# Performance work log

Hardware: AMD Instinct MI355X
Metric: run time of the kernel (lower is better)

Reference implementation:

```python
import jax, jax.numpy as jnp
import numpy as np

B, T, F = 512, 256, 1024


def setup_inputs() -> dict:
    key = jax.random.key(0)
    ks = jax.random.split(key, 8)
    s = 1.0 / np.sqrt(F)
    return {
        "z_state": jax.random.normal(ks[0], (B, F), dtype=jnp.float32),
        "past_predictions": jax.random.normal(ks[1], (B, T, F), dtype=jnp.float32),
        "Wq": jax.random.normal(ks[2], (F, F), dtype=jnp.float32) * s,
        "Wk": jax.random.normal(ks[3], (F, F), dtype=jnp.float32) * s,
        "Wv": jax.random.normal(ks[4], (F, F), dtype=jnp.float32) * s,
        "bq": jnp.zeros((F,), dtype=jnp.float32),
        "bk": jnp.zeros((F,), dtype=jnp.float32),
        "bv": jnp.zeros((F,), dtype=jnp.float32),
    }


def reference(z_state, past_predictions, Wq, Wk, Wv, bq, bk, bv):
    # torch Linear: y = x @ W.T + b  (W is [out, in])
    query = z_state @ Wq.T + bq                         # [B, D]
    keys = jnp.einsum("btf,df->btd", past_predictions, Wk) + bk   # [B, T, D]
    values = jnp.einsum("btf,df->btd", past_predictions, Wv) + bv  # [B, T, D]
    # single-query attention: scores [B, T] (note: no 1/sqrt(d) scaling in source)
    scores = jnp.einsum("bd,btd->bt", query, keys)
    weights = jax.nn.softmax(scores, axis=-1)
    context = jnp.einsum("bt,btd->bd", weights, values)  # [B, D]
    return context
```

## Files before the change

kernel.cpp:

```cpp
#include <hip/hip_runtime.h>
#include <math.h>


#define MM 512
#define NN 1024
#define KK 1024

template<int BT, int SUMA, int BIAS>
__global__ __launch_bounds__(256) void gemm_f32(const float* __restrict__ A,
        const float* __restrict__ Bm, const float* __restrict__ bias,
        float* __restrict__ C)
{
    __shared__ float As[16][68];
    __shared__ float Bs[16][68];
    const int tid = threadIdx.x;
    const int tx = tid & 15, ty = tid >> 4;
    const int n0 = blockIdx.x * 64, m0 = blockIdx.y * 64, kz = blockIdx.z;
    const int kbeg = kz * 512;
    const int arow = tid >> 2, akq = tid & 3;

    float c[4][4] = {};

    for (int kt = 0; kt < 512; kt += 16) {
        const int k0 = kbeg + kt;
        {
            const float* ap = A + (size_t)(m0 + arow) * KK + k0 + akq * 4;
            float4 a = *(const float4*)ap;
            if (SUMA) {
                float4 a2 = *(const float4*)(ap + MM * NN);
                a.x += a2.x; a.y += a2.y; a.z += a2.z; a.w += a2.w;
            }
            As[akq*4+0][arow] = a.x; As[akq*4+1][arow] = a.y;
            As[akq*4+2][arow] = a.z; As[akq*4+3][arow] = a.w;
        }
        if (BT) {
            const float* bp = Bm + (size_t)(n0 + arow) * KK + k0 + akq * 4;
            float4 b = *(const float4*)bp;
            Bs[akq*4+0][arow] = b.x; Bs[akq*4+1][arow] = b.y;
            Bs[akq*4+2][arow] = b.z; Bs[akq*4+3][arow] = b.w;
        } else {
            const int krow = tid >> 4, nq = tid & 15;
            float4 b = *(const float4*)(Bm + (size_t)(k0 + krow) * NN + n0 + nq * 4);
            *(float4*)&Bs[krow][nq * 4] = b;
        }
        __syncthreads();
        #pragma unroll
        for (int k = 0; k < 16; ++k) {
            float4 a4 = *(const float4*)&As[k][ty * 4];
            float4 b4 = *(const float4*)&Bs[k][tx * 4];
            float av[4] = {a4.x, a4.y, a4.z, a4.w};
            float bw[4] = {b4.x, b4.y, b4.z, b4.w};
            #pragma unroll
            for (int i = 0; i < 4; ++i)
                #pragma unroll
                for (int j = 0; j < 4; ++j)
                    c[i][j] = fmaf(av[i], bw[j], c[i][j]);
        }
        __syncthreads();
    }

    float* Cp = C + (size_t)kz * MM * NN;
    #pragma unroll
    for (int i = 0; i < 4; ++i) {
        const int m = m0 + ty * 4 + i;
        const int n = n0 + tx * 4;
        float4 o = make_float4(c[i][0], c[i][1], c[i][2], c[i][3]);
        if (BIAS && kz == 0) {
            o.x += bias[n]; o.y += bias[n+1]; o.z += bias[n+2]; o.w += bias[n+3];
        }
        *(float4*)&Cp[(size_t)m * NN + n] = o;
    }
}

__global__ __launch_bounds__(256) void attn_stream(const float* __restrict__ past,
        const float* __restrict__ qk2, float* __restrict__ ctx)
{
    const int b = blockIdx.x;
    const int e = threadIdx.x;
    const int lane = e & 63, w = e >> 6;
    __shared__ float red[2][4][8];

    const float* qp = qk2 + (size_t)b * 1024 + e * 4;
    float4 q4 = *(const float4*)qp;
    {
        float4 q4b = *(const float4*)(qp + MM * NN);
        q4.x += q4b.x; q4.y += q4b.y; q4.z += q4b.z; q4.w += q4b.w;
    }

    float4 acc = make_float4(0.f, 0.f, 0.f, 0.f);
    float m = -INFINITY, l = 0.f;
    const float* base = past + (size_t)b * 256 * 1024 + e * 4;

    for (int t0 = 0; t0 < 256; t0 += 8) {
        const int buf = (t0 >> 3) & 1;
        float4 r[8];
        float p[8];
        #pragma unroll
        for (int j = 0; j < 8; ++j)
            r[j] = *(const float4*)(base + (size_t)(t0 + j) * 1024);
        #pragma unroll
        for (int j = 0; j < 8; ++j)
            p[j] = q4.x*r[j].x + q4.y*r[j].y + q4.z*r[j].z + q4.w*r[j].w;
        #pragma unroll
        for (int j = 0; j < 8; ++j) {
            #pragma unroll
            for (int off = 1; off < 64; off <<= 1)
                p[j] += __shfl_xor(p[j], off, 64);
        }
        if (lane == 0) {
            #pragma unroll
            for (int j = 0; j < 8; ++j) red[buf][w][j] = p[j];
        }
        __syncthreads();
        float s[8];
        #pragma unroll
        for (int j = 0; j < 8; ++j)
            s[j] = red[buf][0][j] + red[buf][1][j] + red[buf][2][j] + red[buf][3][j];

        float cmax = s[0];
        #pragma unroll
        for (int j = 1; j < 8; ++j) cmax = fmaxf(cmax, s[j]);
        const float mn = fmaxf(m, cmax);
        const float alpha = __expf(m - mn);
        float pe[8], sum = 0.f;
        #pragma unroll
        for (int j = 0; j < 8; ++j) { pe[j] = __expf(s[j] - mn); sum += pe[j]; }
        l = l * alpha + sum;
        acc.x *= alpha; acc.y *= alpha; acc.z *= alpha; acc.w *= alpha;
        #pragma unroll
        for (int j = 0; j < 8; ++j) {
            acc.x = fmaf(pe[j], r[j].x, acc.x);
            acc.y = fmaf(pe[j], r[j].y, acc.y);
            acc.z = fmaf(pe[j], r[j].z, acc.z);
            acc.w = fmaf(pe[j], r[j].w, acc.w);
        }
        m = mn;
    }
    const float inv = 1.0f / l;
    float4 o = make_float4(acc.x * inv, acc.y * inv, acc.z * inv, acc.w * inv);
    *(float4*)(ctx + (size_t)b * 1024 + e * 4) = o;
}

__global__ __launch_bounds__(256) void add_bias_out(const float* __restrict__ o2,
        const float* __restrict__ bv, float* __restrict__ out)
{
    const int i = (blockIdx.x * 256 + threadIdx.x) * 4;
    float4 a = *(const float4*)(o2 + i);
    float4 b = *(const float4*)(o2 + MM * NN + i);
    const int n = i & 1023;
    float4 bb = *(const float4*)(bv + n);
    float4 r = make_float4(a.x + b.x + bb.x, a.y + b.y + bb.y,
                           a.z + b.z + bb.z, a.w + b.w + bb.w);
    *(float4*)(out + i) = r;
}

extern "C" void kernel_launch(void* const* d_in, const int* in_sizes, int n_in,
                              void* d_out, int out_size, void* d_ws, size_t ws_size,
                              hipStream_t stream) {
    const float* z    = (const float*)d_in[0];
    const float* past = (const float*)d_in[1];
    const float* Wq   = (const float*)d_in[2];
    const float* Wk   = (const float*)d_in[3];
    const float* Wv   = (const float*)d_in[4];
    const float* bq   = (const float*)d_in[5];
    const float* bv   = (const float*)d_in[7];
    float* out = (float*)d_out;

    float* q2  = (float*)d_ws;
    float* qk2 = q2 + 2 * MM * NN;
    float* ctx = qk2 + 2 * MM * NN;
    float* o2  = q2;

    dim3 g(NN / 64, MM / 64, 2), blk(256);
    gemm_f32<1, 0, 1><<<g, blk, 0, stream>>>(z,   Wq, bq,      q2);
    gemm_f32<0, 1, 0><<<g, blk, 0, stream>>>(q2,  Wk, nullptr, qk2);
    attn_stream<<<dim3(512), blk, 0, stream>>>(past, qk2, ctx);
    gemm_f32<1, 0, 0><<<g, blk, 0, stream>>>(ctx, Wv, nullptr, o2);
    add_bias_out<<<dim3(512), blk, 0, stream>>>(o2, bv, out);
}
```

Baseline: 795.5 us.

## Split attention over time across wavefronts with split-K combine and wider GEMM K-split

Replaces the one-block-per-batch streaming attention with a split-T design: 2048 blocks, each wavefront handling 16 timesteps independently with a lazy-rescale online softmax and no block-level syncs. A separate combine kernel merges the per-wave partial (m, l, acc) results. The GEMM K-split also rises from 2 to 4 partitions to launch more blocks. The cost is extra partial-result traffic (about 32MB of pacc) and more reduction reads in the consumer kernels.

```diff
diff --git a/kernel.cpp b/kernel.cpp
--- a/kernel.cpp
+++ b/kernel.cpp
@@ -5,6 +5,8 @@
 #define MM 512
 #define NN 1024
 #define KK 1024
+#define NPART 4
+#define KCHUNK (KK / NPART)
 
 template<int BT, int SUMA, int BIAS>
 __global__ __launch_bounds__(256) void gemm_f32(const float* __restrict__ A,
@@ -16,19 +18,22 @@
     const int tid = threadIdx.x;
     const int tx = tid & 15, ty = tid >> 4;
     const int n0 = blockIdx.x * 64, m0 = blockIdx.y * 64, kz = blockIdx.z;
-    const int kbeg = kz * 512;
+    const int kbeg = kz * KCHUNK;
     const int arow = tid >> 2, akq = tid & 3;
 
     float c[4][4] = {};
 
-    for (int kt = 0; kt < 512; kt += 16) {
+    for (int kt = 0; kt < KCHUNK; kt += 16) {
         const int k0 = kbeg + kt;
         {
             const float* ap = A + (size_t)(m0 + arow) * KK + k0 + akq * 4;
             float4 a = *(const float4*)ap;
             if (SUMA) {
-                float4 a2 = *(const float4*)(ap + MM * NN);
-                a.x += a2.x; a.y += a2.y; a.z += a2.z; a.w += a2.w;
+                #pragma unroll
+                for (int p = 1; p < NPART; ++p) {
+                    float4 a2 = *(const float4*)(ap + (size_t)p * MM * NN);
+                    a.x += a2.x; a.y += a2.y; a.z += a2.z; a.w += a2.w;
+                }
             }
             As[akq*4+0][arow] = a.x; As[akq*4+1][arow] = a.y;
             As[akq*4+2][arow] = a.z; As[akq*4+3][arow] = a.w;
@@ -72,73 +77,117 @@
     }
 }
 
-__global__ __launch_bounds__(256) void attn_stream(const float* __restrict__ past,
-        const float* __restrict__ qk2, float* __restrict__ ctx)
+#define TW 16
+
+__global__ __launch_bounds__(256) void attn_part(const float* __restrict__ past,
+        const float* __restrict__ qk2, float* __restrict__ pacc,
+        float2* __restrict__ pml)
+{
+    const int bid = blockIdx.x;
+    const int b = bid >> 2, c = bid & 3;
+    const int lane = threadIdx.x & 63, w = threadIdx.x >> 6;
+    const int widx = (c << 2) | w;
+    const int t0 = widx * TW;
+
+    float4 qk[4];
+    #pragma unroll
+    for (int q = 0; q < 4; ++q) {
+        const float* qp = qk2 + (size_t)b * NN + q * 256 + lane * 4;
+        float4 v = *(const float4*)qp;
+        #pragma unroll
+        for (int p = 1; p < NPART; ++p) {
+            float4 v2 = *(const float4*)(qp + (size_t)p * MM * NN);
+            v.x += v2.x; v.y += v2.y; v.z += v2.z; v.w += v2.w;
+        }
+        qk[q] = v;
+    }
+
+    const float* base = past + ((size_t)b * 256 + t0) * NN + lane * 4;
+    float m = -INFINITY, l = 0.f;
+    float4 acc[4] = {};
+
+    float4 r[4], rn[4];
+    #pragma unroll
+    for (int q = 0; q < 4; ++q) r[q] = *(const float4*)(base + q * 256);
+
+    #pragma unroll 2
+    for (int t = 0; t < TW; ++t) {
+        if (t + 1 < TW) {
+            #pragma unroll
+            for (int q = 0; q < 4; ++q)
+                rn[q] = *(const float4*)(base + (size_t)(t + 1) * NN + q * 256);
+        }
+        const float d0 = r[0].x*qk[0].x + r[0].y*qk[0].y + r[0].z*qk[0].z + r[0].w*qk[0].w;
+        const float d1 = r[1].x*qk[1].x + r[1].y*qk[1].y + r[1].z*qk[1].z + r[1].w*qk[1].w;
+        const float d2 = r[2].x*qk[2].x + r[2].y*qk[2].y + r[2].z*qk[2].z + r[2].w*qk[2].w;
+        const float d3 = r[3].x*qk[3].x + r[3].y*qk[3].y + r[3].z*qk[3].z + r[3].w*qk[3].w;
+        float p = (d0 + d1) + (d2 + d3);
+        #pragma unroll
+        for (int off = 1; off < 64; off <<= 1)
+            p += __shfl_xor(p, off, 64);
+        float dd = p - m;
+        if (dd > 8.f) {
+            const float alpha = __expf(-dd);
+            l *= alpha;
+            #pragma unroll
+            for (int q = 0; q < 4; ++q) {
+                acc[q].x *= alpha; acc[q].y *= alpha;
+                acc[q].z *= alpha; acc[q].w *= alpha;
+            }
+            m = p; dd = 0.f;
+        }
+        const float pe = __expf(dd);
+        l += pe;
+        #pragma unroll
+        for (int q = 0; q < 4; ++q) {
+            acc[q].x = fmaf(pe, r[q].x, acc[q].x);
+            acc[q].y = fmaf(pe, r[q].y, acc[q].y);
+            acc[q].z = fmaf(pe, r[q].z, acc[q].z);
+            acc[q].w = fmaf(pe, r[q].w, acc[q].w);
+        }
+        #pragma unroll
+        for (int q = 0; q < 4; ++q) r[q] = rn[q];
+    }
+
+    float* pa = pacc + ((size_t)b * 16 + widx) * NN + lane * 4;
+    #pragma unroll
+    for (int q = 0; q < 4; ++q) *(float4*)(pa + q * 256) = acc[q];
+    if (lane == 0) pml[b * 16 + widx] = make_float2(m, l);
+}
+
+__global__ __launch_bounds__(256) void attn_combine(const float* __restrict__ pacc,
+        const float2* __restrict__ pml, float* __restrict__ ctx)
 {
     const int b = blockIdx.x;
     const int e = threadIdx.x;
-    const int lane = e & 63, w = e >> 6;
-    __shared__ float red[2][4][8];
-
-    const float* qp = qk2 + (size_t)b * 1024 + e * 4;
-    float4 q4 = *(const float4*)qp;
-    {
-        float4 q4b = *(const float4*)(qp + MM * NN);
-        q4.x += q4b.x; q4.y += q4b.y; q4.z += q4b.z; q4.w += q4b.w;
-    }
-
-    float4 acc = make_float4(0.f, 0.f, 0.f, 0.f);
-    float m = -INFINITY, l = 0.f;
-    const float* base = past + (size_t)b * 256 * 1024 + e * 4;
-
-    for (int t0 = 0; t0 < 256; t0 += 8) {
-        const int buf = (t0 >> 3) & 1;
-        float4 r[8];
-        float p[8];
-        #pragma unroll
-        for (int j = 0; j < 8; ++j)
-            r[j] = *(const float4*)(base + (size_t)(t0 + j) * 1024);
-        #pragma unroll
-        for (int j = 0; j < 8; ++j)
-            p[j] = q4.x*r[j].x + q4.y*r[j].y + q4.z*r[j].z + q4.w*r[j].w;
-        #pragma unroll
-        for (int j = 0; j < 8; ++j) {
-            #pragma unroll
-            for (int off = 1; off < 64; off <<= 1)
-                p[j] += __shfl_xor(p[j], off, 64);
-        }
-        if (lane == 0) {
-            #pragma unroll
-            for (int j = 0; j < 8; ++j) red[buf][w][j] = p[j];
-        }
-        __syncthreads();
-        float s[8];
-        #pragma unroll
-        for (int j = 0; j < 8; ++j)
-            s[j] = red[buf][0][j] + red[buf][1][j] + red[buf][2][j] + red[buf][3][j];
-
-        float cmax = s[0];
-        #pragma unroll
-        for (int j = 1; j < 8; ++j) cmax = fmaxf(cmax, s[j]);
-        const float mn = fmaxf(m, cmax);
-        const float alpha = __expf(m - mn);
-        float pe[8], sum = 0.f;
-        #pragma unroll
-        for (int j = 0; j < 8; ++j) { pe[j] = __expf(s[j] - mn); sum += pe[j]; }
-        l = l * alpha + sum;
-        acc.x *= alpha; acc.y *= alpha; acc.z *= alpha; acc.w *= alpha;
-        #pragma unroll
-        for (int j = 0; j < 8; ++j) {
-            acc.x = fmaf(pe[j], r[j].x, acc.x);
-            acc.y = fmaf(pe[j], r[j].y, acc.y);
-            acc.z = fmaf(pe[j], r[j].z, acc.z);
-            acc.w = fmaf(pe[j], r[j].w, acc.w);
-        }
-        m = mn;
-    }
-    const float inv = 1.0f / l;
-    float4 o = make_float4(acc.x * inv, acc.y * inv, acc.z * inv, acc.w * inv);
-    *(float4*)(ctx + (size_t)b * 1024 + e * 4) = o;
+    __shared__ float sm[16], sl[16];
+    if (e < 16) {
+        float2 v = pml[b * 16 + e];
+        sm[e] = v.x; sl[e] = v.y;
+    }
+    __syncthreads();
+    float M = sm[0];
+    #pragma unroll
+    for (int i = 1; i < 16; ++i) M = fmaxf(M, sm[i]);
+    float L = 0.f, wgt[16];
+    #pragma unroll
+    for (int i = 0; i < 16; ++i) {
+        wgt[i] = __expf(sm[i] - M);
+        L = fmaf(sl[i], wgt[i], L);
+    }
+    const float inv = 1.f / L;
+    const float* pa = pacc + (size_t)b * 16 * NN + e * 4;
+    float4 o = {};
+    #pragma unroll
+    for (int i = 0; i < 16; ++i) {
+        float4 a = *(const float4*)(pa + (size_t)i * NN);
+        o.x = fmaf(wgt[i], a.x, o.x);
+        o.y = fmaf(wgt[i], a.y, o.y);
+        o.z = fmaf(wgt[i], a.z, o.z);
+        o.w = fmaf(wgt[i], a.w, o.w);
+    }
+    o.x *= inv; o.y *= inv; o.z *= inv; o.w *= inv;
+    *(float4*)(ctx + (size_t)b * NN + e * 4) = o;
 }
 
 __global__ __launch_bounds__(256) void add_bias_out(const float* __restrict__ o2,
@@ -146,12 +195,15 @@
 {
     const int i = (blockIdx.x * 256 + threadIdx.x) * 4;
     float4 a = *(const float4*)(o2 + i);
-    float4 b = *(const float4*)(o2 + MM * NN + i);
+    #pragma unroll
+    for (int p = 1; p < NPART; ++p) {
+        float4 b = *(const float4*)(o2 + (size_t)p * MM * NN + i);
+        a.x += b.x; a.y += b.y; a.z += b.z; a.w += b.w;
+    }
     const int n = i & 1023;
     float4 bb = *(const float4*)(bv + n);
-    float4 r = make_float4(a.x + b.x + bb.x, a.y + b.y + bb.y,
-                           a.z + b.z + bb.z, a.w + b.w + bb.w);
-    *(float4*)(out + i) = r;
+    float4 rr = make_float4(a.x + bb.x, a.y + bb.y, a.z + bb.z, a.w + bb.w);
+    *(float4*)(out + i) = rr;
 }
 
 extern "C" void kernel_launch(void* const* d_in, const int* in_sizes, int n_in,
@@ -166,15 +218,18 @@
     const float* bv   = (const float*)d_in[7];
     float* out = (float*)d_out;
 
-    float* q2  = (float*)d_ws;
-    float* qk2 = q2 + 2 * MM * NN;
-    float* ctx = qk2 + 2 * MM * NN;
-    float* o2  = q2;
-
-    dim3 g(NN / 64, MM / 64, 2), blk(256);
+    float* q2   = (float*)d_ws;
+    float* qk2  = q2 + (size_t)NPART * MM * NN;
+    float* ctx  = qk2 + (size_t)NPART * MM * NN;
+    float* pacc = ctx + (size_t)MM * NN;
+    float2* pml = (float2*)(pacc + (size_t)512 * 16 * 1024);
+    float* o2   = q2;
+
+    dim3 g(NN / 64, MM / 64, NPART), blk(256);
     gemm_f32<1, 0, 1><<<g, blk, 0, stream>>>(z,   Wq, bq,      q2);
     gemm_f32<0, 1, 0><<<g, blk, 0, stream>>>(q2,  Wk, nullptr, qk2);
-    attn_stream<<<dim3(512), blk, 0, stream>>>(past, qk2, ctx);
+    attn_part<<<dim3(2048), blk, 0, stream>>>(past, qk2, pacc, pml);
+    attn_combine<<<dim3(512), blk, 0, stream>>>(pacc, pml, ctx);
     gemm_f32<1, 0, 0><<<g, blk, 0, stream>>>(ctx, Wv, nullptr, o2);
     add_bias_out<<<dim3(512), blk, 0, stream>>>(o2, bv, out);
 }
```

After: 785.3 us. About the same (-1.3%).
